# Kernel optimization log

Measured on AMD Instinct MI355X. Metric: run time of the kernel, lower is better.

The kernel has to match this reference:

```python
import jax, jax.numpy as jnp
import numpy as np

B, C, F, T = 4, 64, 128, 128
K = 8        # kernel_size
H = 32       # lstm hidden size
L = 4        # lstm layers
EPS = 1e-5


def setup_inputs() -> dict:
    key = jax.random.key(0)
    ks = jax.random.split(key, 12)
    f = lambda k, s: jax.random.normal(k, s, dtype=jnp.float32) * 0.1
    return dict(
        x=jax.random.normal(ks[0], (B, C, F, T), dtype=jnp.float32),
        gamma=jnp.ones((C,), jnp.float32),
        beta=jnp.zeros((C,), jnp.float32),
        # layer 0 (input size C*K), stacked over 2 directions
        w_ih0=f(ks[1], (2, 4 * H, C * K)),
        w_hh0=f(ks[2], (2, 4 * H, H)),
        b_ih0=f(ks[3], (2, 4 * H)),
        b_hh0=f(ks[4], (2, 4 * H)),
        # layers 1..L-1 (input size 2*H), stacked [L-1, 2dirs, ...]
        w_ih=f(ks[5], (L - 1, 2, 4 * H, 2 * H)),
        w_hh=f(ks[6], (L - 1, 2, 4 * H, H)),
        b_ih=f(ks[7], (L - 1, 2, 4 * H)),
        b_hh=f(ks[8], (L - 1, 2, 4 * H)),
        # ConvTranspose1d weight, torch layout [in=2H, out=C, K]
        wct=f(ks[9], (2 * H, C, K)),
        bct=f(ks[10], (C,)),
    )


def _lstm_dir(gx, whh, reverse):
    # gx: [S, N, 4H] precomputed input projections (+ both biases)
    Hh = whh.shape[1]
    N = gx.shape[1]

    def step(carry, g):
        h, c = carry
        g = g + h @ whh.T
        i, fg, gg, o = jnp.split(g, 4, axis=-1)  # torch gate order i,f,g,o
        c = jax.nn.sigmoid(fg) * c + jax.nn.sigmoid(i) * jnp.tanh(gg)
        h = jax.nn.sigmoid(o) * jnp.tanh(c)
        return (h, c), h

    init = (jnp.zeros((N, Hh), gx.dtype), jnp.zeros((N, Hh), gx.dtype))
    _, hs = jax.lax.scan(step, init, gx, reverse=reverse)
    return hs  # [S, N, H], time-aligned with input


def _bilstm(xs, wih, whh, bih, bhh):
    outs = []
    for d, rev in ((0, False), (1, True)):
        gx = jnp.einsum('sni,gi->sng', xs, wih[d]) + bih[d] + bhh[d]
        outs.append(_lstm_dir(gx, whh[d], rev))
    return jnp.concatenate(outs, axis=-1)  # [S, N, 2H]


def reference(x, gamma, beta, w_ih0, w_hh0, b_ih0, b_hh0,
              w_ih, w_hh, b_ih, b_hh, wct, bct):
    x = jnp.swapaxes(x, -1, -2)  # [B, C, T, F]
    res = x
    Bb, Cc, Tt, Ff = x.shape
    # InstanceNorm2d (affine, biased variance over (T,F))
    mu = jnp.mean(x, axis=(2, 3), keepdims=True)
    var = jnp.var(x, axis=(2, 3), keepdims=True)
    xn = (x - mu) * jax.lax.rsqrt(var + EPS)
    xn = xn * gamma[None, :, None, None] + beta[None, :, None, None]
    # [B,F,C,T] -> [B*F, C, T]
    xf = jnp.transpose(xn, (0, 3, 1, 2)).reshape(Bb * Ff, Cc, Tt)
    # unfold(dim=2, size=K, step=1): [BF, C, T', K]
    Tp = Tt - K + 1
    idx = jnp.arange(Tp)[:, None] + jnp.arange(K)[None, :]
    seq = jnp.transpose(xf[:, :, idx], (2, 0, 1, 3)).reshape(Tp, Bb * Ff, Cc * K)
    # 4-layer bidirectional LSTM
    h = _bilstm(seq, w_ih0, w_hh0, b_ih0, b_hh0)
    for l in range(w_ih.shape[0]):
        h = _bilstm(h, w_ih[l], w_hh[l], b_ih[l], b_hh[l])
    # [S, BF, 2H] -> [BF, 2H, S]
    h = jnp.transpose(h, (1, 2, 0))
    # ConvTranspose1d stride=1, pad=0: out length = S + K - 1 = T
    y = jax.lax.conv_transpose(
        h, wct, strides=(1,), padding='VALID',
        dimension_numbers=('NCH', 'IOH', 'NCH'), transpose_kernel=True)
    y = y + bct[None, :, None]
    y = y.reshape(Bb, Ff, Cc, Tt)
    y = jnp.transpose(y, (0, 2, 3, 1)) + res  # [B, C, T, F]
    return jnp.swapaxes(y, -1, -2)  # back to [B, C, F, T]
```

## Files before the change

kernel.cpp:

```cpp
#include <hip/hip_runtime.h>

#define B_ 4
#define C_ 64
#define F_ 128
#define T_ 128
#define K_ 8
#define H_ 32
#define S_ 121
#define N_ 512
#define G_ 128
#define CK_ 512

typedef __attribute__((ext_vector_type(8))) short short8;
typedef __attribute__((ext_vector_type(4))) float f32x4;
union FragU { uint4 u; short8 s; };

__device__ __forceinline__ unsigned int pk2(float a, float b){
  unsigned int ua = __float_as_uint(a); ua += 0x7fffu + ((ua>>16)&1u);
  unsigned int ub = __float_as_uint(b); ub += 0x7fffu + ((ub>>16)&1u);
  return (ua>>16) | (ub & 0xffff0000u);
}
__device__ __forceinline__ unsigned short bfu(float a){
  unsigned int ua = __float_as_uint(a); ua += 0x7fffu + ((ua>>16)&1u);
  return (unsigned short)(ua>>16);
}

__device__ __forceinline__ int gslot(int g){ return ((g & 63) << 1) | (g >> 6); }

__global__ __launch_bounds__(256) void k_norm(const float* __restrict__ x,
    const float* __restrict__ gamma, const float* __restrict__ beta,
    float* __restrict__ scale, float* __restrict__ shift){
  int bc = blockIdx.x;
  const float* p = x + (size_t)bc * (F_*T_);
  float s = 0.f, q = 0.f;
  for (int i = threadIdx.x; i < F_*T_; i += 256){ float v = p[i]; s += v; q += v*v; }
  #pragma unroll
  for (int o = 32; o; o >>= 1){ s += __shfl_down(s, o); q += __shfl_down(q, o); }
  __shared__ float ss[4], qq[4];
  int w = threadIdx.x >> 6;
  if ((threadIdx.x & 63) == 0){ ss[w] = s; qq[w] = q; }
  __syncthreads();
  if (threadIdx.x == 0){
    s = ss[0]+ss[1]+ss[2]+ss[3]; q = qq[0]+qq[1]+qq[2]+qq[3];
    float mu  = s / (float)(F_*T_);
    float var = q / (float)(F_*T_) - mu*mu;
    if (var < 0.f) var = 0.f;
    int c = bc & (C_-1);
    float sc = gamma[c] * rsqrtf(var + 1e-5f);
    scale[bc] = sc;
    shift[bc] = beta[c] - mu * sc;
  }
}

__global__ __launch_bounds__(256) void k_wcvt(const float* __restrict__ a,
    unsigned short* __restrict__ o, int nel){
  int i = blockIdx.x*256 + threadIdx.x;
  if (i < nel) o[i] = bfu(a[i]);
}
__global__ __launch_bounds__(256) void k_wrev(const float* __restrict__ a,
    unsigned short* __restrict__ o, int nel){
  int i = blockIdx.x*256 + threadIdx.x;
  if (i < nel){ int j = (i & ~7) | (7 - (i & 7)); o[i] = bfu(a[j]); }
}

__global__ __launch_bounds__(256) void k_gx0(const float* __restrict__ x,
    const float* __restrict__ scale, const float* __restrict__ shift,
    const unsigned short* __restrict__ wb0, const float* __restrict__ bi,
    const float* __restrict__ bh, unsigned short* __restrict__ gx){
  __shared__ unsigned int xsp[C_][80];
  int n = blockIdx.x >> 1, half = blockIdx.x & 1;
  int b = n >> 7, f = n & 127;
  const float* xb = x + (size_t)b*C_*F_*T_ + (size_t)f*T_;
  for (int i = threadIdx.x; i < C_*72; i += 256){
    int c = i / 72, j = i - c*72;
    int t0 = half*64 + j;
    float sc = scale[b*C_+c], sh = shift[b*C_+c];
    float v0 = (t0   < T_) ? xb[(size_t)c*F_*T_ + t0  ]*sc + sh : 0.f;
    float v1 = (t0+1 < T_) ? xb[(size_t)c*F_*T_ + t0+1]*sc + sh : 0.f;
    xsp[c][j] = pk2(v0, v1);
  }
  __syncthreads();
  int lane = threadIdx.x & 63, wv = threadIdx.x >> 6;
  int ln = lane & 15, quad = lane >> 4;
  int g256[4]; f32x4 acc[4][4];
  #pragma unroll
  for (int gi = 0; gi < 4; ++gi){
    g256[gi] = (wv*4 + gi)*16 + ln;
    float bv = bi[g256[gi]] + bh[g256[gi]];
    #pragma unroll
    for (int stl = 0; stl < 4; ++stl) acc[stl][gi] = (f32x4){bv, bv, bv, bv};
  }
  FragU bcur[4], bnxt[4];
  #pragma unroll
  for (int gi = 0; gi < 4; ++gi)
    bcur[gi].u = *(const uint4*)(wb0 + (size_t)g256[gi]*CK_ + quad*8);
  for (int kb = 0; kb < 16; ++kb){
    if (kb < 15){
      #pragma unroll
      for (int gi = 0; gi < 4; ++gi)
        bnxt[gi].u = *(const uint4*)(wb0 + (size_t)g256[gi]*CK_ + (kb+1)*32 + quad*8);
    }
    #pragma unroll
    for (int stl = 0; stl < 4; ++stl){
      FragU a;
      const unsigned int* rp = &xsp[kb*4 + quad][stl*16 + ln];
      a.u.x = rp[0]; a.u.y = rp[2]; a.u.z = rp[4]; a.u.w = rp[6];
      #pragma unroll
      for (int gi = 0; gi < 4; ++gi)
        acc[stl][gi] = __builtin_amdgcn_mfma_f32_16x16x32_bf16(a.s, bcur[gi].s, acc[stl][gi], 0, 0, 0);
    }
    #pragma unroll
    for (int gi = 0; gi < 4; ++gi) bcur[gi] = bnxt[gi];
  }
  #pragma unroll
  for (int stl = 0; stl < 4; ++stl)
    #pragma unroll
    for (int gi = 0; gi < 4; ++gi){
      int d = g256[gi] >> 7, g = g256[gi] & 127;
      #pragma unroll
      for (int r = 0; r < 4; ++r){
        int s = (half*4 + stl)*16 + quad*4 + r;
        if (s < S_)
          gx[((size_t)(d*N_ + n)*S_ + s)*G_ + gslot(g)] = bfu(acc[stl][gi][r]);
      }
    }
}

__global__ __launch_bounds__(128)
__attribute__((amdgpu_waves_per_eu(1, 1)))
void k_mega(const unsigned short* __restrict__ gx,
    const float* __restrict__ whh0,
    const unsigned short* __restrict__ wlb,
    const float* __restrict__ bih, const float* __restrict__ bhh,
    const float* __restrict__ whh,
    unsigned short* __restrict__ hout){
  __shared__ unsigned int rawA[64][68];
  __shared__ unsigned int rawB[64][68];
  __shared__ unsigned int glds[2][32][66];
  __shared__ unsigned int hsp[32][136];

  int n = blockIdx.x;
  int tid = threadIdx.x;
  int lane = tid & 63, d = tid >> 6;
  int j = lane & 31, hi = lane >> 5;
  int ln = lane & 15, quad = lane >> 4;

  float w1[32], w2[32];
  float hv = 0.f, c = 0.f;
  unsigned int hgd[4];
  auto rl = [&](int k)->float{
    return __uint_as_float(__builtin_amdgcn_readlane(__float_as_uint(hv), k));
  };
  auto step = [&](unsigned int cur, int u){
    float acc1 = __uint_as_float(cur << 16);
    float acc2 = __uint_as_float(cur & 0xffff0000u);
    float s1a = acc1, s1b = 0.f, s1c = 0.f, s1d = 0.f;
    float s2a = acc2, s2b = 0.f, s2c = 0.f, s2d = 0.f;
    #pragma unroll
    for (int k = 0; k < 32; k += 4){
      float h0 = rl(k), h1 = rl(k+1), h2 = rl(k+2), h3 = rl(k+3);
      s1a += h0*w1[k];   s1b += h1*w1[k+1]; s1c += h2*w1[k+2]; s1d += h3*w1[k+3];
      s2a += h0*w2[k];   s2b += h1*w2[k+1]; s2c += h2*w2[k+2]; s2d += h3*w2[k+3];
    }
    acc1 = (s1a + s1b) + (s1c + s1d);
    acc2 = (s2a + s2b) + (s2c + s2d);
    float a1 = 1.f/(1.f + __expf(-acc1));
    float x2 = hi ? acc2 : 2.f*acc2;
    float tt = 1.f/(1.f + __expf(-x2));
    float a2 = hi ? tt : 2.f*tt - 1.f;
    float b1 = __shfl_xor(a1, 32);
    float b2 = __shfl_xor(a2, 32);
    float i_ = hi ? b1 : a1;
    float f_ = hi ? a1 : b1;
    float g_ = hi ? b2 : a2;
    float o_ = hi ? a2 : b2;
    c = f_*c + i_*g_;
    float tc = 1.f/(1.f + __expf(-2.f*c));
    hv = o_*(2.f*tc - 1.f);
    unsigned int hb = (unsigned int)bfu(hv);
    if ((u & 1) == 0) hgd[u >> 1] = hb;
    else              hgd[u >> 1] |= hb << 16;
  };
  auto loadw = [&](const float* wr1, const float* wr2){
    #pragma unroll
    for (int q = 0; q < 8; ++q){
      float4 aa = *(const float4*)(wr1 + q*4);
      float4 bb = *(const float4*)(wr2 + q*4);
      w1[q*4+0]=aa.x; w1[q*4+1]=aa.y; w1[q*4+2]=aa.z; w1[q*4+3]=aa.w;
      w2[q*4+0]=bb.x; w2[q*4+1]=bb.y; w2[q*4+2]=bb.z; w2[q*4+3]=bb.w;
    }
    #pragma unroll
    for (int k = 0; k < 32; ++k){
      asm volatile("" : "+v"(w1[k]));
      asm volatile("" : "+v"(w2[k]));
    }
  };

  {
    loadw(whh0 + (size_t)(d*G_ + lane)*H_, whh0 + (size_t)(d*G_ + lane + 64)*H_);
    const unsigned int* gxu = (const unsigned int*)gx;
    ptrdiff_t stride = d ? -64 : 64;
    const unsigned int* p0 = gxu + ((size_t)(d*N_ + n)*S_ + (d ? (S_-1) : 0))*64 + lane;
    unsigned short* hrow = (unsigned short*)&rawA[d*32 + j][0];
    unsigned int bufA[8], bufB[8];
    #pragma unroll
    for (int u = 0; u < 8; ++u) bufA[u] = p0[stride*u];
    for (int gg = 0; gg < 7; ++gg){
      int g0 = gg*2;
      #pragma unroll
      for (int u = 0; u < 8; ++u) bufB[u] = p0[stride*(8*(g0+1) + u)];
      #pragma unroll
      for (int u = 0; u < 8; ++u) step(bufA[u], u);
      if (!hi) *(uint4*)(hrow + 8*g0) = (uint4){hgd[0], hgd[1], hgd[2], hgd[3]};
      #pragma unroll
      for (int u = 0; u < 8; ++u) bufA[u] = p0[stride*(8*(g0+2) + u)];
      #pragma unroll
      for (int u = 0; u < 8; ++u) step(bufB[u], u);
      if (!hi) *(uint4*)(hrow + 8*(g0+1)) = (uint4){hgd[0], hgd[1], hgd[2], hgd[3]};
    }
    bufB[0] = p0[stride*120];
    #pragma unroll
    for (int u = 0; u < 8; ++u) step(bufA[u], u);
    if (!hi) *(uint4*)(hrow + 112) = (uint4){hgd[0], hgd[1], hgd[2], hgd[3]};
    step(bufB[0], 0);
    if (!hi) hrow[120] = (unsigned short)(hgd[0] & 0xffffu);
  }
  __syncthreads();

  unsigned int (*rin)[68]  = rawA;
  unsigned int (*rout)[68] = rawB;
  for (int l = 0; l < 3; ++l){
    const unsigned short* rawu = (const unsigned short*)&rin[0][0];
    for (int i = tid; i < 32*128; i += 128){
      int srow = i >> 5, ip = i & 31;
      unsigned int v = 0;
      if (srow <= 120){
        int st = (ip < 16) ? srow : (120 - srow);
        v = (unsigned int)rawu[(2*ip)*136 + st] | ((unsigned int)rawu[(2*ip+1)*136 + st] << 16);
      }
      hsp[ip][srow] = v;
    }
    __syncthreads();

    const unsigned short* wp = wlb + (size_t)((l*2 + d)*G_)*64;
    float bias[8];
    const float* bip = bih + (size_t)(l*2 + d)*G_;
    const float* bhp = bhh + (size_t)(l*2 + d)*G_;
    #pragma unroll
    for (int gt = 0; gt < 8; ++gt) bias[gt] = bip[gt*16 + ln] + bhp[gt*16 + ln];
    loadw(whh + (size_t)((l*2 + d)*G_ + lane)*H_,
          whh + (size_t)((l*2 + d)*G_ + lane + 64)*H_);

    FragU bfrc[8][2];
    #pragma unroll
    for (int gt = 0; gt < 8; ++gt){
      bfrc[gt][0].u = *(const uint4*)(wp + (size_t)(gt*16 + ln)*64 + quad*8);
      bfrc[gt][1].u = *(const uint4*)(wp + (size_t)(gt*16 + ln)*64 + 32 + quad*8);
    }

    unsigned short* hrow = (unsigned short*)&rout[d*32 + j][0];
    const unsigned int* gr = &glds[d][0][lane];
    hv = 0.f; c = 0.f;

    for (int ch = 0; ch < 4; ++ch){
      int c0 = d ? (89 - 32*ch) : (32*ch);
      FragU af[2][2];
      #pragma unroll
      for (int stl = 0; stl < 2; ++stl){
        int srow = c0 + stl*16 + ln; if (srow < 0) srow = 0;
        #pragma unroll
        for (int kb = 0; kb < 2; ++kb){
          int ipb = kb*16 + quad*4;
          af[stl][kb].u.x = hsp[ipb+0][srow];
          af[stl][kb].u.y = hsp[ipb+1][srow];
          af[stl][kb].u.z = hsp[ipb+2][srow];
          af[stl][kb].u.w = hsp[ipb+3][srow];
        }
      }
      #pragma unroll
      for (int stl = 0; stl < 2; ++stl)
        #pragma unroll
        for (int gt2 = 0; gt2 < 4; ++gt2){
          f32x4 alo = (f32x4){bias[gt2],   bias[gt2],   bias[gt2],   bias[gt2]};
          f32x4 ahi = (f32x4){bias[gt2+4], bias[gt2+4], bias[gt2+4], bias[gt2+4]};
          alo = __builtin_amdgcn_mfma_f32_16x16x32_bf16(af[stl][0].s, bfrc[gt2  ][0].s, alo, 0, 0, 0);
          alo = __builtin_amdgcn_mfma_f32_16x16x32_bf16(af[stl][1].s, bfrc[gt2  ][1].s, alo, 0, 0, 0);
          ahi = __builtin_amdgcn_mfma_f32_16x16x32_bf16(af[stl][0].s, bfrc[gt2+4][0].s, ahi, 0, 0, 0);
          ahi = __builtin_amdgcn_mfma_f32_16x16x32_bf16(af[stl][1].s, bfrc[gt2+4][1].s, ahi, 0, 0, 0);
          #pragma unroll
          for (int r = 0; r < 4; ++r){
            int off = stl*16 + quad*4 + r;
            int ul = d ? (31 - off) : off;
            glds[d][ul][gt2*16 + ln] = pk2(alo[r], ahi[r]);
          }
        }
      asm volatile("" ::: "memory");
      int nfull = (ch < 3) ? 4 : 3;
      for (int gq = 0; gq < nfull; ++gq){
        unsigned int bv[8];
        #pragma unroll
        for (int u = 0; u < 8; ++u) bv[u] = gr[(gq*8 + u)*66];
        #pragma unroll
        for (int u = 0; u < 8; ++u) step(bv[u], u);
        if (!hi) *(uint4*)(hrow + ch*32 + gq*8) = (uint4){hgd[0], hgd[1], hgd[2], hgd[3]};
      }
      if (ch == 3){
        unsigned int bv0 = gr[24*66];
        step(bv0, 0);
        if (!hi) hrow[120] = (unsigned short)(hgd[0] & 0xffffu);
      }
      asm volatile("" ::: "memory");
    }
    __syncthreads();
    unsigned int (*t)[68] = rin; rin = rout; rout = t;
  }

  unsigned int* ho = (unsigned int*)hout + (size_t)n*64*64;
  for (int i = tid; i < 64*64; i += 128){
    int ci = i >> 6, k = i & 63;
    ho[ci*64 + k] = rin[ci][k];
  }
}

__global__ __launch_bounds__(256) void k_conv(const unsigned short* __restrict__ hin,
    const unsigned short* __restrict__ wA, const float* __restrict__ bct,
    const float* __restrict__ x, float* __restrict__ out){
  __shared__ unsigned int hrawL[64][65];
  __shared__ unsigned int hp2[64][144];
  int n = blockIdx.x, b = n >> 7, f = n & 127;
  const unsigned int* hu = (const unsigned int*)hin + (size_t)n*64*64;
  for (int i = threadIdx.x; i < 64*64; i += 256){
    int ci = i >> 6, k = i & 63;
    hrawL[ci][k] = hu[ci*64 + k];
  }
  __syncthreads();
  const unsigned short* rawu = (const unsigned short*)&hrawL[0][0];
  for (int it = threadIdx.x; it < 64*136; it += 256){
    int ci = it / 136, col = it - ci*136;
    int t0 = col - 8;
    int i0 = (ci < 32) ? t0 : (120 - t0);
    int i1 = (ci < 32) ? (t0+1) : (119 - t0);
    unsigned int lo  = (t0   >= 0 && t0   <= 120) ? rawu[ci*130 + i0] : 0u;
    unsigned int hi2 = (t0+1 >= 0 && t0+1 <= 120) ? rawu[ci*130 + i1] : 0u;
    hp2[ci][col] = lo | (hi2 << 16);
  }
  __syncthreads();
  int lane = threadIdx.x & 63, wv = threadIdx.x >> 6;
  int ln = lane & 15, quad = lane >> 4;
  const unsigned short* wp = wA + (size_t)(wv*16 + ln)*512;
  f32x4 acc[8];
  #pragma unroll
  for (int nt = 0; nt < 8; ++nt) acc[nt] = (f32x4){0.f,0.f,0.f,0.f};
  for (int kb = 0; kb < 16; ++kb){
    FragU afr; afr.u = *(const uint4*)(wp + kb*32 + quad*8);
    int ci = kb*4 + quad;
    #pragma unroll
    for (int nt = 0; nt < 8; ++nt){
      FragU bfr;
      const unsigned int* rp = &hp2[ci][nt*16 + ln + 1];
      bfr.u.x = rp[0]; bfr.u.y = rp[2]; bfr.u.z = rp[4]; bfr.u.w = rp[6];
      acc[nt] = __builtin_amdgcn_mfma_f32_16x16x32_bf16(afr.s, bfr.s, acc[nt], 0, 0, 0);
    }
  }
  float bb[4];
  #pragma unroll
  for (int r = 0; r < 4; ++r) bb[r] = bct[wv*16 + quad*4 + r];
  #pragma unroll
  for (int nt = 0; nt < 8; ++nt)
    #pragma unroll
    for (int r = 0; r < 4; ++r){
      int co = wv*16 + quad*4 + r, t = nt*16 + ln;
      size_t idx = ((size_t)(b*64 + co)*128 + f)*128 + t;
      out[idx] = acc[nt][r] + bb[r] + x[idx];
    }
}

extern "C" void kernel_launch(void* const* d_in, const int* in_sizes, int n_in,
                              void* d_out, int out_size, void* d_ws, size_t ws_size,
                              hipStream_t stream){
  const float* x     = (const float*)d_in[0];
  const float* gamma = (const float*)d_in[1];
  const float* beta  = (const float*)d_in[2];
  const float* wih0  = (const float*)d_in[3];
  const float* whh0  = (const float*)d_in[4];
  const float* bih0  = (const float*)d_in[5];
  const float* bhh0  = (const float*)d_in[6];
  const float* wih   = (const float*)d_in[7];
  const float* whh   = (const float*)d_in[8];
  const float* bih   = (const float*)d_in[9];
  const float* bhh   = (const float*)d_in[10];
  const float* wct   = (const float*)d_in[11];
  const float* bct   = (const float*)d_in[12];
  float* out = (float*)d_out;

  char* wsb = (char*)d_ws;
  float*          scale = (float*)(wsb);
  float*          shift = (float*)(wsb + 1024);
  unsigned short* gx    = (unsigned short*)(wsb + 2048);
  unsigned short* hA    = (unsigned short*)(wsb + 31721472);
  unsigned short* wb0   = (unsigned short*)(wsb + 48498688);
  unsigned short* wlb   = (unsigned short*)(wsb + 48760832);
  unsigned short* wcv   = (unsigned short*)(wsb + 48859136);

  k_norm<<<256, 256, 0, stream>>>(x, gamma, beta, scale, shift);
  k_wcvt<<<512, 256, 0, stream>>>(wih0, wb0, 2*G_*CK_);
  k_wcvt<<<192, 256, 0, stream>>>(wih,  wlb, 3*2*G_*64);
  k_wrev<<<128, 256, 0, stream>>>(wct,  wcv, 64*512);
  k_gx0 <<<1024, 256, 0, stream>>>(x, scale, shift, wb0, bih0, bhh0, gx);
  k_mega<<<512, 128, 0, stream>>>(gx, whh0, wlb, bih, bhh, whh, hA);
  k_conv<<<512, 256, 0, stream>>>(hA, wcv, bct, x, out);
}
```

Measured before the change: 371.2 us.

## Vectorize LSTM recurrence with packed FMA and permlane32 swap; float4 gx0 staging

The recurrent h@Whh dot products in the mega kernel now hold weights as float2 pairs, so the compiler can emit packed FP32 FMAs (v_pk_fma_f32) and issue half as many FMA instructions per step. The cross-half gate exchange moves from two __shfl_xor calls to the permlane32_swap builtin, which avoids LDS-based shuffles on the serial critical path. Separately, the gx0 input staging loads four time samples with one float4 load plus one scalar, and builds four packed bf16 pairs per thread instead of one pair from two scalar loads. The risks are changed summation order in the dot product and the permlane32_swap semantics, which must produce the right i/f/g/o assignment on both lane halves.

```diff
diff --git a/kernel.cpp b/kernel.cpp
--- a/kernel.cpp
+++ b/kernel.cpp
@@ -13,6 +13,8 @@
 
 typedef __attribute__((ext_vector_type(8))) short short8;
 typedef __attribute__((ext_vector_type(4))) float f32x4;
+typedef __attribute__((ext_vector_type(2))) float f32x2;
+typedef __attribute__((ext_vector_type(2))) unsigned int ui2;
 union FragU { uint4 u; short8 s; };
 
 __device__ __forceinline__ unsigned int pk2(float a, float b){
@@ -71,13 +73,23 @@
   int n = blockIdx.x >> 1, half = blockIdx.x & 1;
   int b = n >> 7, f = n & 127;
   const float* xb = x + (size_t)b*C_*F_*T_ + (size_t)f*T_;
-  for (int i = threadIdx.x; i < C_*72; i += 256){
-    int c = i / 72, j = i - c*72;
-    int t0 = half*64 + j;
+  for (int i = threadIdx.x; i < C_*18; i += 256){
+    int c = i / 18, q = i - c*18;
+    int t0 = half*64 + q*4;
     float sc = scale[b*C_+c], sh = shift[b*C_+c];
-    float v0 = (t0   < T_) ? xb[(size_t)c*F_*T_ + t0  ]*sc + sh : 0.f;
-    float v1 = (t0+1 < T_) ? xb[(size_t)c*F_*T_ + t0+1]*sc + sh : 0.f;
-    xsp[c][j] = pk2(v0, v1);
+    const float* xr = xb + (size_t)c*F_*T_;
+    float4 v = (float4){0.f,0.f,0.f,0.f};
+    float e = 0.f;
+    bool in4 = (t0 < T_);
+    if (in4) v = *(const float4*)(xr + t0);
+    if (t0 + 4 < T_) e = xr[t0 + 4];
+    float u0 = in4 ? v.x*sc+sh : 0.f;
+    float u1 = in4 ? v.y*sc+sh : 0.f;
+    float u2 = in4 ? v.z*sc+sh : 0.f;
+    float u3 = in4 ? v.w*sc+sh : 0.f;
+    float u4 = (t0+4 < T_) ? e*sc+sh : 0.f;
+    unsigned int* xc = &xsp[c][q*4];
+    xc[0] = pk2(u0,u1); xc[1] = pk2(u1,u2); xc[2] = pk2(u2,u3); xc[3] = pk2(u3,u4);
   }
   __syncthreads();
   int lane = threadIdx.x & 63, wv = threadIdx.x >> 6;
@@ -145,35 +157,36 @@
   int j = lane & 31, hi = lane >> 5;
   int ln = lane & 15, quad = lane >> 4;
 
-  float w1[32], w2[32];
+  f32x2 w1[16], w2[16];
   float hv = 0.f, c = 0.f;
   unsigned int hgd[4];
   auto rl = [&](int k)->float{
     return __uint_as_float(__builtin_amdgcn_readlane(__float_as_uint(hv), k));
   };
   auto step = [&](unsigned int cur, int u){
-    float acc1 = __uint_as_float(cur << 16);
-    float acc2 = __uint_as_float(cur & 0xffff0000u);
-    float s1a = acc1, s1b = 0.f, s1c = 0.f, s1d = 0.f;
-    float s2a = acc2, s2b = 0.f, s2c = 0.f, s2d = 0.f;
-    #pragma unroll
-    for (int k = 0; k < 32; k += 4){
-      float h0 = rl(k), h1 = rl(k+1), h2 = rl(k+2), h3 = rl(k+3);
-      s1a += h0*w1[k];   s1b += h1*w1[k+1]; s1c += h2*w1[k+2]; s1d += h3*w1[k+3];
-      s2a += h0*w2[k];   s2b += h1*w2[k+1]; s2c += h2*w2[k+2]; s2d += h3*w2[k+3];
-    }
-    acc1 = (s1a + s1b) + (s1c + s1d);
-    acc2 = (s2a + s2b) + (s2c + s2d);
+    float gg1 = __uint_as_float(cur << 16);
+    float gg2 = __uint_as_float(cur & 0xffff0000u);
+    f32x2 A1 = {gg1, 0.f}, B1 = {0.f, 0.f};
+    f32x2 A2 = {gg2, 0.f}, B2 = {0.f, 0.f};
+    #pragma unroll
+    for (int m = 0; m < 16; m += 2){
+      f32x2 h0; h0.x = rl(2*m);   h0.y = rl(2*m+1);
+      f32x2 h1; h1.x = rl(2*m+2); h1.y = rl(2*m+3);
+      A1 += h0*w1[m];   A2 += h0*w2[m];
+      B1 += h1*w1[m+1]; B2 += h1*w2[m+1];
+    }
+    float acc1 = (A1.x + B1.x) + (A1.y + B1.y);
+    float acc2 = (A2.x + B2.x) + (A2.y + B2.y);
     float a1 = 1.f/(1.f + __expf(-acc1));
     float x2 = hi ? acc2 : 2.f*acc2;
     float tt = 1.f/(1.f + __expf(-x2));
     float a2 = hi ? tt : 2.f*tt - 1.f;
-    float b1 = __shfl_xor(a1, 32);
-    float b2 = __shfl_xor(a2, 32);
-    float i_ = hi ? b1 : a1;
-    float f_ = hi ? a1 : b1;
-    float g_ = hi ? b2 : a2;
-    float o_ = hi ? a2 : b2;
+    ui2 p1 = __builtin_amdgcn_permlane32_swap(__float_as_uint(a1), __float_as_uint(a1), false, false);
+    ui2 p2 = __builtin_amdgcn_permlane32_swap(__float_as_uint(a2), __float_as_uint(a2), false, false);
+    float i_ = __uint_as_float(p1.x);
+    float f_ = __uint_as_float(p1.y);
+    float g_ = __uint_as_float(p2.x);
+    float o_ = __uint_as_float(p2.y);
     c = f_*c + i_*g_;
     float tc = 1.f/(1.f + __expf(-2.f*c));
     hv = o_*(2.f*tc - 1.f);
@@ -186,11 +199,11 @@
     for (int q = 0; q < 8; ++q){
       float4 aa = *(const float4*)(wr1 + q*4);
       float4 bb = *(const float4*)(wr2 + q*4);
-      w1[q*4+0]=aa.x; w1[q*4+1]=aa.y; w1[q*4+2]=aa.z; w1[q*4+3]=aa.w;
-      w2[q*4+0]=bb.x; w2[q*4+1]=bb.y; w2[q*4+2]=bb.z; w2[q*4+3]=bb.w;
-    }
-    #pragma unroll
-    for (int k = 0; k < 32; ++k){
+      w1[q*2+0] = (f32x2){aa.x, aa.y}; w1[q*2+1] = (f32x2){aa.z, aa.w};
+      w2[q*2+0] = (f32x2){bb.x, bb.y}; w2[q*2+1] = (f32x2){bb.z, bb.w};
+    }
+    #pragma unroll
+    for (int k = 0; k < 16; ++k){
       asm volatile("" : "+v"(w1[k]));
       asm volatile("" : "+v"(w2[k]));
     }
```

After: 339.7 us. 1.09x faster.
